# Optimization experiments

Measured on AMD Instinct MI355X. Metric: run time of the kernel, lower is better.

The kernel has to match this reference:

```python
import jax, jax.numpy as jnp
import numpy as np

N = 20000
IN_CH = 256
HID = 32
HEADS = 8
OUT_CH = 40
NEG_SLOPE = 0.2


def _gat_layer(x, src, dst, W, a_src, a_dst, b, heads, ch, concat):
    # x: [N, F_in], W: [F_in, heads*ch], a_src/a_dst: [heads, ch], b: [heads*ch] or [ch]
    n = x.shape[0]
    h = (x @ W).reshape(n, heads, ch)                      # [N, H, C]
    alpha_s = jnp.einsum('nhc,hc->nh', h, a_src)           # [N, H]
    alpha_d = jnp.einsum('nhc,hc->nh', h, a_dst)           # [N, H]
    e = jax.nn.leaky_relu(alpha_s[src] + alpha_d[dst], NEG_SLOPE)  # [E, H]
    # segment softmax over edges sharing the same destination node
    m = jax.ops.segment_max(e, dst, num_segments=n)        # [N, H]
    ex = jnp.exp(e - m[dst])                               # [E, H]
    denom = jax.ops.segment_sum(ex, dst, num_segments=n)   # [N, H]
    alpha = ex / (denom[dst] + 1e-16)                      # [E, H]
    out = jax.ops.segment_sum(h[src] * alpha[:, :, None], dst, num_segments=n)  # [N, H, C]
    out = out.reshape(n, heads * ch) if concat else out.mean(axis=1)
    return out + b


def setup_inputs() -> dict:
    key = jax.random.key(0)
    ks = jax.random.split(key, 12)
    x = jax.random.normal(ks[0], (N, IN_CH), dtype=jnp.float32)
    edge_index = jax.random.randint(ks[1], (2, 320000), 0, N, dtype=jnp.int64)
    s1 = 1.0 / np.sqrt(IN_CH)
    s2 = 1.0 / np.sqrt(HEADS * HID)
    W1 = jax.random.uniform(ks[2], (IN_CH, HEADS * HID), jnp.float32, -s1, s1)
    a1_src = jax.random.uniform(ks[3], (HEADS, HID), jnp.float32, -s2, s2)
    a1_dst = jax.random.uniform(ks[4], (HEADS, HID), jnp.float32, -s2, s2)
    b1 = jnp.zeros((HEADS * HID,), jnp.float32)
    W2 = jax.random.uniform(ks[5], (HEADS * HID, OUT_CH), jnp.float32, -s2, s2)
    so = 1.0 / np.sqrt(OUT_CH)
    a2_src = jax.random.uniform(ks[6], (1, OUT_CH), jnp.float32, -so, so)
    a2_dst = jax.random.uniform(ks[7], (1, OUT_CH), jnp.float32, -so, so)
    b2 = jnp.zeros((OUT_CH,), jnp.float32)
    return {"x": x, "edge_index": edge_index, "W1": W1, "a1_src": a1_src,
            "a1_dst": a1_dst, "b1": b1, "W2": W2, "a2_src": a2_src,
            "a2_dst": a2_dst, "b2": b2}


def reference(x, edge_index, W1, a1_src, a1_dst, b1, W2, a2_src, a2_dst, b2):
    n = x.shape[0]
    loop = jnp.arange(n, dtype=edge_index.dtype)
    src = jnp.concatenate([edge_index[0], loop])  # PyG adds self-loops by default
    dst = jnp.concatenate([edge_index[1], loop])
    # dropout layers are identity in eval mode
    h = _gat_layer(x, src, dst, W1, a1_src, a1_dst, b1, HEADS, HID, concat=True)
    h = jax.nn.elu(h)
    out = _gat_layer(h, src, dst, W2, a2_src, a2_dst, b2, 1, OUT_CH, concat=False)
    return jax.nn.log_softmax(out, axis=1)
```

## Files before the change

### kernel.cpp

```cpp
#include <hip/hip_runtime.h>
#include <math.h>

#define N_NODES 20000
#define E_RAW   320000
#define E_TOT   (E_RAW + N_NODES)
#define IN_CH   256
#define HEADS   8
#define HID     32
#define HH      (HEADS*HID)
#define OUT_CH  40
#define NC2     48
#define NEG     0.2f
#define CSTRIDE 64

#define ZB_BLKS   79
#define HIST_BLKS ((E_TOT + 255) / 256)
#define G1_BLKS   313
#define N_PAD     20032

typedef __attribute__((ext_vector_type(8))) short  short8;
typedef __attribute__((ext_vector_type(4))) float  floatx4;

__device__ __forceinline__ unsigned short f2bf(float f) {
    unsigned int u = __float_as_uint(f);
    unsigned int r = (u + 0x7FFFu + ((u >> 16) & 1u)) >> 16;
    return (unsigned short)r;
}
__device__ __forceinline__ float bf2f(unsigned short h) {
    return __uint_as_float(((unsigned int)h) << 16);
}
__device__ __forceinline__ float lexp(float v) {
    v = (v > 0.f) ? v : NEG * v;
    return __expf(v);
}

__device__ __forceinline__ void gload16(const void* g, void* l) {
    __builtin_amdgcn_global_load_lds(
        (const __attribute__((address_space(1))) void*)g,
        (__attribute__((address_space(3))) void*)l, 16, 0, 0);
}


__global__ void setup_prep(const float* __restrict__ W1,
                           const float* __restrict__ W2,
                           unsigned short* __restrict__ w1t,
                           unsigned short* __restrict__ w2t,
                           int* __restrict__ deg) {
    int b = blockIdx.x;
    int t = threadIdx.x;
    if (b < ZB_BLKS) {
        int i = b * 256 + t;
        if (i < N_NODES) deg[i] = 0;
    } else if (b < ZB_BLKS + HH) {
        int c = b - ZB_BLKS;
        w1t[c * IN_CH + t] = f2bf(W1[(size_t)t * HH + c]);
    } else {
        int c = b - ZB_BLKS - HH;
        w2t[c * HH + t] = (c < OUT_CH) ? f2bf(W2[(size_t)t * OUT_CH + c]) : (unsigned short)0;
    }
}

__global__ __launch_bounds__(256) void gemm1(const float* __restrict__ x,
                                             const unsigned short* __restrict__ w1t,
                                             const float* __restrict__ a1s,
                                             const float* __restrict__ a1d,
                                             unsigned short* __restrict__ h1b,
                                             float* __restrict__ as1,
                                             float* __restrict__ ad1,
                                             const int* __restrict__ ei,
                                             int* __restrict__ deg,
                                             int* __restrict__ csr) {
    __shared__ unsigned char Al[64 * 512];
    __shared__ unsigned char Bl[256 * 128];
    int t = threadIdx.x;

    if (blockIdx.x >= G1_BLKS) {
        int e = (blockIdx.x - G1_BLKS) * 256 + t;
        if (e < E_TOT) {
            int s, d;
            if (e < E_RAW) { s = ei[e]; d = ei[E_RAW + e]; }
            else           { s = e - E_RAW; d = s; }
            int slot = atomicAdd(&deg[d], 1);
            if (slot < CSTRIDE) csr[d * CSTRIDE + slot] = s;
        }
        return;
    }

    int wave = t >> 6, lane = t & 63;
    int ln = lane & 15, q = lane >> 4;
    int n0 = blockIdx.x * 64;
    const char* bbase = (const char*)w1t;

    #pragma unroll
    for (int j = 0; j < 8; j++) {
        int R = (wave * 8 + j) * 1024;
        int o = R + lane * 16;
        int r = o >> 7;
        int cb = (o & 127) ^ ((r & 7) << 4);
        gload16(bbase + (size_t)r * 512 + cb, &Bl[R]);
    }

    {
        int srow = t >> 4, scol = t & 15;
        #pragma unroll
        for (int pp = 0; pp < 4; pp++) {
            int row = srow + pp * 16;
            int n = n0 + row;
            #pragma unroll
            for (int kc = 0; kc < 4; kc++) {
                float4 v = (n < N_NODES)
                    ? *reinterpret_cast<const float4*>(&x[(size_t)n * IN_CH + kc * 64 + scol * 4])
                    : make_float4(0.f, 0.f, 0.f, 0.f);
                ushort4 pv;
                pv.x = f2bf(v.x); pv.y = f2bf(v.y); pv.z = f2bf(v.z); pv.w = f2bf(v.w);
                int bo = row * 512 + ((kc * 128 + scol * 8) ^ ((row & 7) << 4));
                *reinterpret_cast<ushort4*>(&Al[bo]) = pv;
            }
        }
    }
    __syncthreads();

    floatx4 acc[16];
    #pragma unroll
    for (int f = 0; f < 16; f++) acc[f] = (floatx4){0.f, 0.f, 0.f, 0.f};

    int xorv = (ln & 7) << 4;

    for (int c = 0; c < 4; c++) {
        #pragma unroll
        for (int ks = 0; ks < 2; ks++) {
            int ao = (16 * wave + ln) * 512 + c * 128 + ((ks * 64 + q * 16) ^ xorv);
            short8 a = *reinterpret_cast<const short8*>(&Al[ao]);
            int bo0 = ln * 128 + ((ks * 64 + q * 16) ^ xorv);
            #pragma unroll
            for (int f = 0; f < 16; f++) {
                short8 bfr = *reinterpret_cast<const short8*>(&Bl[bo0 + f * 2048]);
                acc[f] = __builtin_amdgcn_mfma_f32_16x16x32_bf16(a, bfr, acc[f], 0, 0, 0);
            }
        }
        if (c < 3) {
            __syncthreads();
            #pragma unroll
            for (int j = 0; j < 8; j++) {
                int R = (wave * 8 + j) * 1024;
                int o = R + lane * 16;
                int r = o >> 7;
                int cb = (o & 127) ^ ((r & 7) << 4);
                gload16(bbase + (size_t)r * 512 + (c + 1) * 128 + cb, &Bl[R]);
            }
            __syncthreads();
        }
    }

    float Asr[16], Adr[16];
    #pragma unroll
    for (int f = 0; f < 16; f++) {
        Asr[f] = a1s[16 * f + ln];
        Adr[f] = a1d[16 * f + ln];
    }
    #pragma unroll
    for (int f = 0; f < 16; f++) {
        #pragma unroll
        for (int r = 0; r < 4; r++) {
            int n = n0 + 16 * wave + q * 4 + r;
            if (n < N_NODES)
                h1b[(size_t)n * HH + 16 * f + ln] = f2bf(acc[f][r]);
        }
    }
    #pragma unroll
    for (int lh = 0; lh < 8; lh++) {
        #pragma unroll
        for (int r = 0; r < 4; r++) {
            float ps = acc[2*lh][r] * Asr[2*lh] + acc[2*lh+1][r] * Asr[2*lh+1];
            float pd = acc[2*lh][r] * Adr[2*lh] + acc[2*lh+1][r] * Adr[2*lh+1];
            ps += __shfl_xor(ps, 1); ps += __shfl_xor(ps, 2);
            ps += __shfl_xor(ps, 4); ps += __shfl_xor(ps, 8);
            pd += __shfl_xor(pd, 1); pd += __shfl_xor(pd, 2);
            pd += __shfl_xor(pd, 4); pd += __shfl_xor(pd, 8);
            int n = n0 + 16 * wave + q * 4 + r;
            if (ln == 0 && n < N_NODES) {
                as1[n * HEADS + lh] = ps;
                ad1[n * HEADS + lh] = pd;
            }
        }
    }
}


__global__ __launch_bounds__(256) void aggr1(const unsigned short* __restrict__ h1b,
                                             const float* __restrict__ as1,
                                             const float* __restrict__ ad1,
                                             const float* __restrict__ b1,
                                             const int* __restrict__ degv,
                                             const int* __restrict__ csr,
                                             unsigned short* __restrict__ h2b) {
    int d = blockIdx.x * 4 + (threadIdx.x >> 6);
    int lane = threadIdx.x & 63;
    int h = lane >> 3;
    int c4 = lane * 4;
    int start = d * CSTRIDE;
    int deg = degv[d];
    deg = (deg > CSTRIDE) ? CSTRIDE : deg;
    float adv = ad1[d * HEADS + h];

    float a0 = 0.f, a1 = 0.f, a2 = 0.f, a3 = 0.f, den = 0.f;
    int jj = 0;
    for (; jj + 8 <= deg; jj += 8) {
        int s[8];
        #pragma unroll
        for (int i = 0; i < 8; i++) s[i] = csr[start + jj + i];
        float e[8];
        #pragma unroll
        for (int i = 0; i < 8; i++) e[i] = as1[s[i] * HEADS + h];
        ushort4 pv[8];
        #pragma unroll
        for (int i = 0; i < 8; i++)
            pv[i] = *reinterpret_cast<const ushort4*>(&h1b[(size_t)s[i] * HH + c4]);
        #pragma unroll
        for (int i = 0; i < 8; i++) {
            float w = lexp(e[i] + adv);
            den += w;
            a0 = fmaf(bf2f(pv[i].x), w, a0);
            a1 = fmaf(bf2f(pv[i].y), w, a1);
            a2 = fmaf(bf2f(pv[i].z), w, a2);
            a3 = fmaf(bf2f(pv[i].w), w, a3);
        }
    }
    for (; jj < deg; jj++) {
        int s = csr[start + jj];
        float w = lexp(as1[s * HEADS + h] + adv);
        den += w;
        ushort4 pv = *reinterpret_cast<const ushort4*>(&h1b[(size_t)s * HH + c4]);
        a0 = fmaf(bf2f(pv.x), w, a0);
        a1 = fmaf(bf2f(pv.y), w, a1);
        a2 = fmaf(bf2f(pv.z), w, a2);
        a3 = fmaf(bf2f(pv.w), w, a3);
    }
    float inv = 1.0f / (den + 1e-16f);
    float4 bv = *reinterpret_cast<const float4*>(&b1[c4]);
    float r0 = a0 * inv + bv.x;
    float r1 = a1 * inv + bv.y;
    float r2 = a2 * inv + bv.z;
    float r3 = a3 * inv + bv.w;
    r0 = (r0 > 0.f) ? r0 : (__expf(r0) - 1.f);
    r1 = (r1 > 0.f) ? r1 : (__expf(r1) - 1.f);
    r2 = (r2 > 0.f) ? r2 : (__expf(r2) - 1.f);
    r3 = (r3 > 0.f) ? r3 : (__expf(r3) - 1.f);
    ushort4 ov;
    ov.x = f2bf(r0); ov.y = f2bf(r1); ov.z = f2bf(r2); ov.w = f2bf(r3);
    *reinterpret_cast<ushort4*>(&h2b[(size_t)d * HH + c4]) = ov;
}


__global__ __launch_bounds__(256) void gemm2(const unsigned short* __restrict__ h2b,
                                             const unsigned short* __restrict__ w2t,
                                             const float* __restrict__ a2s,
                                             const float* __restrict__ a2d,
                                             unsigned short* __restrict__ h3b,
                                             float* __restrict__ as2,
                                             float* __restrict__ ad2) {
    __shared__ unsigned char Al[64 * 512];
    __shared__ unsigned char Bl[NC2 * 512];
    int t = threadIdx.x;
    int wave = t >> 6, lane = t & 63;
    int ln = lane & 15, q = lane >> 4;
    int n0 = blockIdx.x * 64;
    const char* abase = (const char*)h2b + (size_t)n0 * 512;
    const char* bbase = (const char*)w2t;

    #pragma unroll
    for (int j = 0; j < 8; j++) {
        int R = (wave * 8 + j) * 1024;
        int o = R + lane * 16;
        int r = o >> 9;
        int cb = (o & 511) ^ ((r & 7) << 4);
        gload16(abase + (size_t)r * 512 + cb, &Al[R]);
    }
    #pragma unroll
    for (int j = 0; j < 6; j++) {
        int R = (wave * 6 + j) * 1024;
        int o = R + lane * 16;
        int r = o >> 9;
        int cb = (o & 511) ^ ((r & 7) << 4);
        gload16(bbase + (size_t)r * 512 + cb, &Bl[R]);
    }
    __syncthreads();

    floatx4 acc[3];
    #pragma unroll
    for (int f = 0; f < 3; f++) acc[f] = (floatx4){0.f, 0.f, 0.f, 0.f};

    int xorv = (ln & 7) << 4;

    #pragma unroll
    for (int kf = 0; kf < 8; kf++) {
        int ao = ((16 * wave + ln) * 512 + kf * 64 + q * 16) ^ xorv;
        short8 a = *reinterpret_cast<const short8*>(&Al[ao]);
        int bo0 = (ln * 512 + kf * 64 + q * 16) ^ xorv;
        #pragma unroll
        for (int f = 0; f < 3; f++) {
            short8 bfr = *reinterpret_cast<const short8*>(&Bl[bo0 + f * 8192]);
            acc[f] = __builtin_amdgcn_mfma_f32_16x16x32_bf16(a, bfr, acc[f], 0, 0, 0);
        }
    }

    float a2sv[3], a2dv[3];
    #pragma unroll
    for (int f = 0; f < 3; f++) {
        int c = 16 * f + ln;
        a2sv[f] = (c < OUT_CH) ? a2s[c] : 0.f;
        a2dv[f] = (c < OUT_CH) ? a2d[c] : 0.f;
    }
    #pragma unroll
    for (int r = 0; r < 4; r++) {
        int n = n0 + 16 * wave + q * 4 + r;
        float ps = acc[0][r] * a2sv[0] + acc[1][r] * a2sv[1] + acc[2][r] * a2sv[2];
        float pd = acc[0][r] * a2dv[0] + acc[1][r] * a2dv[1] + acc[2][r] * a2dv[2];
        ps += __shfl_xor(ps, 1); ps += __shfl_xor(ps, 2);
        ps += __shfl_xor(ps, 4); ps += __shfl_xor(ps, 8);
        pd += __shfl_xor(pd, 1); pd += __shfl_xor(pd, 2);
        pd += __shfl_xor(pd, 4); pd += __shfl_xor(pd, 8);
        if (n < N_NODES) {
            #pragma unroll
            for (int f = 0; f < 3; f++) {
                int c = 16 * f + ln;
                if (c < OUT_CH)
                    h3b[(size_t)n * OUT_CH + c] = f2bf(acc[f][r]);
            }
            if (ln == 0) { as2[n] = ps; ad2[n] = pd; }
        }
    }
}


__global__ __launch_bounds__(256) void aggr2(const unsigned short* __restrict__ h3b,
                                             const float* __restrict__ as2,
                                             const float* __restrict__ ad2,
                                             const float* __restrict__ b2,
                                             const int* __restrict__ degv,
                                             const int* __restrict__ csr,
                                             float* __restrict__ out) {
    int d = blockIdx.x * 4 + (threadIdx.x >> 6);
    int lane = threadIdx.x & 63;
    int start = d * CSTRIDE;
    int deg = degv[d];
    deg = (deg > CSTRIDE) ? CSTRIDE : deg;
    float adv = ad2[d];
    bool ok = (lane < OUT_CH);
    int cl = ok ? lane : 0;

    float acc = 0.f, den = 0.f;
    int jj = 0;
    for (; jj + 8 <= deg; jj += 8) {
        int s[8];
        #pragma unroll
        for (int i = 0; i < 8; i++) s[i] = csr[start + jj + i];
        float e[8];
        #pragma unroll
        for (int i = 0; i < 8; i++) e[i] = as2[s[i]];
        unsigned short qv[8];
        #pragma unroll
        for (int i = 0; i < 8; i++) qv[i] = h3b[(size_t)s[i] * OUT_CH + cl];
        #pragma unroll
        for (int i = 0; i < 8; i++) {
            float w = lexp(e[i] + adv);
            den += w;
            acc = fmaf(bf2f(qv[i]), w, acc);
        }
    }
    for (; jj < deg; jj++) {
        int s = csr[start + jj];
        float w = lexp(as2[s] + adv);
        den += w;
        acc = fmaf(bf2f(h3b[(size_t)s * OUT_CH + cl]), w, acc);
    }

    float r = ok ? (acc / (den + 1e-16f) + b2[lane]) : -1e30f;
    float mx = r;
    #pragma unroll
    for (int off = 32; off >= 1; off >>= 1) mx = fmaxf(mx, __shfl_xor(mx, off));
    float ex = ok ? __expf(r - mx) : 0.f;
    float se = ex;
    #pragma unroll
    for (int off = 32; off >= 1; off >>= 1) se += __shfl_xor(se, off);
    if (ok) out[(size_t)d * OUT_CH + lane] = r - mx - __logf(se);
}


extern "C" void kernel_launch(void* const* d_in, const int* in_sizes, int n_in,
                              void* d_out, int out_size, void* d_ws, size_t ws_size,
                              hipStream_t stream) {
    const float* x   = (const float*)d_in[0];
    const int*   ei  = (const int*)  d_in[1];
    const float* W1  = (const float*)d_in[2];
    const float* a1s = (const float*)d_in[3];
    const float* a1d = (const float*)d_in[4];
    const float* b1  = (const float*)d_in[5];
    const float* W2  = (const float*)d_in[6];
    const float* a2s = (const float*)d_in[7];
    const float* a2d = (const float*)d_in[8];
    const float* b2  = (const float*)d_in[9];
    float* out = (float*)d_out;

    char* p = (char*)d_ws;
    auto alloc = [&](size_t bytes) {
        char* r = p;
        p += (bytes + 255) & ~(size_t)255;
        return r;
    };
    unsigned short* h1b = (unsigned short*)alloc((size_t)N_NODES * HH * 2);
    unsigned short* h2b = (unsigned short*)alloc((size_t)N_PAD * HH * 2);
    unsigned short* h3b = (unsigned short*)alloc((size_t)N_NODES * OUT_CH * 2);
    unsigned short* w1t = (unsigned short*)alloc((size_t)IN_CH * HH * 2);
    unsigned short* w2t = (unsigned short*)alloc((size_t)NC2 * HH * 2);
    float* as1  = (float*)alloc((size_t)N_NODES * HEADS * 4);
    float* ad1  = (float*)alloc((size_t)N_NODES * HEADS * 4);
    float* as2v = (float*)alloc((size_t)N_NODES * 4);
    float* ad2v = (float*)alloc((size_t)N_NODES * 4);
    int* deg    = (int*)alloc((size_t)N_NODES * 4);
    int* csr    = (int*)alloc((size_t)N_NODES * CSTRIDE * 4);

    setup_prep<<<ZB_BLKS + HH + NC2, 256, 0, stream>>>(W1, W2, w1t, w2t, deg);
    gemm1<<<G1_BLKS + HIST_BLKS, 256, 0, stream>>>(x, w1t, a1s, a1d, h1b, as1, ad1,
                                                   ei, deg, csr);
    aggr1<<<N_NODES / 4, 256, 0, stream>>>(h1b, as1, ad1, b1, deg, csr, h2b);
    gemm2<<<313, 256, 0, stream>>>(h2b, w2t, a2s, a2d, h3b, as2v, ad2v);
    aggr2<<<N_NODES / 4, 256, 0, stream>>>(h3b, as2v, ad2v, b2, deg, csr, out);
}
```

Measured before the change: 159.1 us.

## Halve gemm1 row tile and add x cache-warming pass in setup kernel

The gemm1 tile drops from 64 to 32 rows per block, doubling the block count. Each wave now covers 16 rows by 128 columns with 8 accumulators instead of 16 rows by 256, which cuts registers and LDS and should raise occupancy. The x-row bounds checks are removed since 20000 divides evenly by 32. setup_prep gains 2500 blocks that read all of x and discard it, to warm the cache before gemm1 runs; this adds a full pass over x and extra launch work.

Result: no change. 161.3 us (+1.4%).

```diff
diff --git a/kernel.cpp b/kernel.cpp
--- a/kernel.cpp
+++ b/kernel.cpp
@@ -14,8 +14,9 @@
 #define CSTRIDE 64
 
 #define ZB_BLKS   79
+#define XW_BLKS   2500
 #define HIST_BLKS ((E_TOT + 255) / 256)
-#define G1_BLKS   313
+#define G1_BLKS   625
 #define N_PAD     20032
 
 typedef __attribute__((ext_vector_type(8))) short  short8;
@@ -41,7 +42,8 @@
 }
 
 
-__global__ void setup_prep(const float* __restrict__ W1,
+__global__ void setup_prep(const float* __restrict__ x,
+                           const float* __restrict__ W1,
                            const float* __restrict__ W2,
                            unsigned short* __restrict__ w1t,
                            unsigned short* __restrict__ w2t,
@@ -54,9 +56,17 @@
     } else if (b < ZB_BLKS + HH) {
         int c = b - ZB_BLKS;
         w1t[c * IN_CH + t] = f2bf(W1[(size_t)t * HH + c]);
-    } else {
+    } else if (b < ZB_BLKS + HH + NC2) {
         int c = b - ZB_BLKS - HH;
         w2t[c * HH + t] = (c < OUT_CH) ? f2bf(W2[(size_t)t * OUT_CH + c]) : (unsigned short)0;
+    } else {
+        int bb = b - (ZB_BLKS + HH + NC2);
+        int n = bb * 8 + (t >> 5);
+        int c0 = (t & 31) * 8;
+        const float4* src = reinterpret_cast<const float4*>(&x[(size_t)n * IN_CH + c0]);
+        float4 v0 = src[0], v1 = src[1];
+        float s = v0.x + v0.y + v0.z + v0.w + v1.x + v1.y + v1.z + v1.w;
+        asm volatile("" :: "v"(s));
     }
 }
 
@@ -70,7 +80,7 @@
                                              const int* __restrict__ ei,
                                              int* __restrict__ deg,
                                              int* __restrict__ csr) {
-    __shared__ unsigned char Al[64 * 512];
+    __shared__ unsigned char Al[32 * 512];
     __shared__ unsigned char Bl[256 * 128];
     int t = threadIdx.x;
 
@@ -88,7 +98,8 @@
 
     int wave = t >> 6, lane = t & 63;
     int ln = lane & 15, q = lane >> 4;
-    int n0 = blockIdx.x * 64;
+    int rg = wave & 1, cg = wave >> 1;
+    int n0 = blockIdx.x * 32;
     const char* bbase = (const char*)w1t;
 
     #pragma unroll
@@ -101,39 +112,34 @@
     }
 
     {
-        int srow = t >> 4, scol = t & 15;
-        #pragma unroll
-        for (int pp = 0; pp < 4; pp++) {
-            int row = srow + pp * 16;
-            int n = n0 + row;
+        int row = t >> 3;
+        int cseg = (t & 7) * 32;
+        int n = n0 + row;
+        #pragma unroll
+        for (int kc = 0; kc < 8; kc++) {
+            float4 v = *reinterpret_cast<const float4*>(&x[(size_t)n * IN_CH + cseg + kc * 4]);
+            ushort4 pv;
+            pv.x = f2bf(v.x); pv.y = f2bf(v.y); pv.z = f2bf(v.z); pv.w = f2bf(v.w);
+            int bo = row * 512 + ((cseg * 2 + kc * 8) ^ ((row & 7) << 4));
+            *reinterpret_cast<ushort4*>(&Al[bo]) = pv;
+        }
+    }
+    __syncthreads();
+
+    floatx4 acc[8];
+    #pragma unroll
+    for (int f = 0; f < 8; f++) acc[f] = (floatx4){0.f, 0.f, 0.f, 0.f};
+
+    int xorv = (ln & 7) << 4;
+
+    for (int c = 0; c < 4; c++) {
+        #pragma unroll
+        for (int ks = 0; ks < 2; ks++) {
+            int ao = (16 * rg + ln) * 512 + c * 128 + ((ks * 64 + q * 16) ^ xorv);
+            short8 a = *reinterpret_cast<const short8*>(&Al[ao]);
+            int bo0 = cg * 16384 + ln * 128 + ((ks * 64 + q * 16) ^ xorv);
             #pragma unroll
-            for (int kc = 0; kc < 4; kc++) {
-                float4 v = (n < N_NODES)
-                    ? *reinterpret_cast<const float4*>(&x[(size_t)n * IN_CH + kc * 64 + scol * 4])
-                    : make_float4(0.f, 0.f, 0.f, 0.f);
-                ushort4 pv;
-                pv.x = f2bf(v.x); pv.y = f2bf(v.y); pv.z = f2bf(v.z); pv.w = f2bf(v.w);
-                int bo = row * 512 + ((kc * 128 + scol * 8) ^ ((row & 7) << 4));
-                *reinterpret_cast<ushort4*>(&Al[bo]) = pv;
-            }
-        }
-    }
-    __syncthreads();
-
-    floatx4 acc[16];
-    #pragma unroll
-    for (int f = 0; f < 16; f++) acc[f] = (floatx4){0.f, 0.f, 0.f, 0.f};
-
-    int xorv = (ln & 7) << 4;
-
-    for (int c = 0; c < 4; c++) {
-        #pragma unroll
-        for (int ks = 0; ks < 2; ks++) {
-            int ao = (16 * wave + ln) * 512 + c * 128 + ((ks * 64 + q * 16) ^ xorv);
-            short8 a = *reinterpret_cast<const short8*>(&Al[ao]);
-            int bo0 = ln * 128 + ((ks * 64 + q * 16) ^ xorv);
-            #pragma unroll
-            for (int f = 0; f < 16; f++) {
+            for (int f = 0; f < 8; f++) {
                 short8 bfr = *reinterpret_cast<const short8*>(&Bl[bo0 + f * 2048]);
                 acc[f] = __builtin_amdgcn_mfma_f32_16x16x32_bf16(a, bfr, acc[f], 0, 0, 0);
             }
@@ -152,23 +158,22 @@
         }
     }
 
-    float Asr[16], Adr[16];
-    #pragma unroll
-    for (int f = 0; f < 16; f++) {
-        Asr[f] = a1s[16 * f + ln];
-        Adr[f] = a1d[16 * f + ln];
-    }
-    #pragma unroll
-    for (int f = 0; f < 16; f++) {
+    float Asr[8], Adr[8];
+    #pragma unroll
+    for (int f = 0; f < 8; f++) {
+        Asr[f] = a1s[cg * 128 + 16 * f + ln];
+        Adr[f] = a1d[cg * 128 + 16 * f + ln];
+    }
+    #pragma unroll
+    for (int f = 0; f < 8; f++) {
         #pragma unroll
         for (int r = 0; r < 4; r++) {
-            int n = n0 + 16 * wave + q * 4 + r;
-            if (n < N_NODES)
-                h1b[(size_t)n * HH + 16 * f + ln] = f2bf(acc[f][r]);
-        }
-    }
-    #pragma unroll
-    for (int lh = 0; lh < 8; lh++) {
+            int n = n0 + 16 * rg + q * 4 + r;
+            h1b[(size_t)n * HH + cg * 128 + 16 * f + ln] = f2bf(acc[f][r]);
+        }
+    }
+    #pragma unroll
+    for (int lh = 0; lh < 4; lh++) {
         #pragma unroll
         for (int r = 0; r < 4; r++) {
             float ps = acc[2*lh][r] * Asr[2*lh] + acc[2*lh+1][r] * Asr[2*lh+1];
@@ -177,10 +182,10 @@
             ps += __shfl_xor(ps, 4); ps += __shfl_xor(ps, 8);
             pd += __shfl_xor(pd, 1); pd += __shfl_xor(pd, 2);
             pd += __shfl_xor(pd, 4); pd += __shfl_xor(pd, 8);
-            int n = n0 + 16 * wave + q * 4 + r;
-            if (ln == 0 && n < N_NODES) {
-                as1[n * HEADS + lh] = ps;
-                ad1[n * HEADS + lh] = pd;
+            int n = n0 + 16 * rg + q * 4 + r;
+            if (ln == 0) {
+                as1[n * HEADS + cg * 4 + lh] = ps;
+                ad1[n * HEADS + cg * 4 + lh] = pd;
             }
         }
     }
@@ -420,7 +425,8 @@
     int* deg    = (int*)alloc((size_t)N_NODES * 4);
     int* csr    = (int*)alloc((size_t)N_NODES * CSTRIDE * 4);
 
-    setup_prep<<<ZB_BLKS + HH + NC2, 256, 0, stream>>>(W1, W2, w1t, w2t, deg);
+    setup_prep<<<ZB_BLKS + HH + NC2 + XW_BLKS, 256, 0, stream>>>(
+        x, W1, W2, w1t, w2t, deg);
     gemm1<<<G1_BLKS + HIST_BLKS, 256, 0, stream>>>(x, w1t, a1s, a1d, h1b, as1, ad1,
                                                    ei, deg, csr);
     aggr1<<<N_NODES / 4, 256, 0, stream>>>(h1b, as1, ad1, b1, deg, csr, h2b);
```
